# Performance work log

Hardware: AMD Instinct MI355X
Metric: run time of the kernel (lower is better)

Reference implementation:

```python
import jax, jax.numpy as jnp
import numpy as np

B, S, UNITS = 32, 2048, 512
D = 2 * UNITS  # 1024


def setup_inputs() -> dict:
    key = jax.random.key(0)
    ks = jax.random.split(key, 12)
    s = 1.0 / np.sqrt(D)
    mask = (jax.random.uniform(ks[0], (B, S)) < 0.9).astype(jnp.float32)
    mask = mask.at[:, 0].set(1.0)  # guarantee no all-zero row
    return {
        "dec_hidden": jax.random.normal(ks[1], (2, B, UNITS), dtype=jnp.float32),
        "enc_output": jax.random.normal(ks[2], (B, S, D), dtype=jnp.float32),
        "enc_pad_mask": mask,
        "prev_coverage": jax.random.uniform(ks[3], (B, S), dtype=jnp.float32) * 0.1,
        "Wh": jax.random.uniform(ks[4], (D, D), minval=-s, maxval=s),
        "bh": jax.random.uniform(ks[5], (D,), minval=-s, maxval=s),
        "Ws": jax.random.uniform(ks[6], (D, D), minval=-s, maxval=s),
        "bs": jax.random.uniform(ks[7], (D,), minval=-s, maxval=s),
        "Wc": jax.random.uniform(ks[8], (D, 1), minval=-1.0, maxval=1.0),
        "bc": jax.random.uniform(ks[9], (D,), minval=-1.0, maxval=1.0),
        "v": jax.random.uniform(ks[10], (1, D), minval=-s, maxval=s),
        "bv": jax.random.uniform(ks[11], (1,), minval=-s, maxval=s),
        "use_coverage": 1,
    }


def reference(dec_hidden, enc_output, enc_pad_mask, prev_coverage,
              Wh, bh, Ws, bs, Wc, bc, v, bv, use_coverage):
    # dec_hidden: (2, B, units) -> (B, 1, 2*units)
    dec = jnp.transpose(dec_hidden, (1, 0, 2)).reshape(dec_hidden.shape[1], 1, -1)
    enc_features = jnp.einsum('bsd,ed->bse', enc_output, Wh) + bh  # (B,S,D)
    dec_features = jnp.einsum('bod,ed->boe', dec, Ws) + bs          # (B,1,D)
    att_inputs = enc_features + dec_features
    if use_coverage:
        # Linear(1 -> D) applied to prev_coverage[..., None]
        coverage_features = prev_coverage[:, :, None] * Wc[:, 0][None, None, :] + bc
        att_inputs = att_inputs + coverage_features
    score = jnp.einsum('bsd,od->bso', jnp.tanh(att_inputs), v) + bv  # (B,S,1)
    attention_weights = jax.nn.softmax(score, axis=1)[..., 0]        # (B,S)
    attention_weights = attention_weights * enc_pad_mask
    attention_weights = attention_weights / jnp.sum(attention_weights, axis=1, keepdims=True)
    context_vector = jnp.einsum('bs,bsd->bd', attention_weights, enc_output)
    if use_coverage:
        coverage_vector = prev_coverage + attention_weights
        return context_vector, attention_weights, coverage_vector
    return context_vector, attention_weights
```

## Files before the change

kernel.cpp:

```cpp
#include <hip/hip_runtime.h>
#include <hip/hip_bf16.h>

#define BATCH 32
#define SEQ   2048
#define DIM   1024

typedef __attribute__((ext_vector_type(4))) float f32x4;
typedef __attribute__((ext_vector_type(8))) short short8;

static __device__ __forceinline__ ushort f2bf(float x) {
    __hip_bfloat16 h = __float2bfloat16(x);
    union { __hip_bfloat16 h; ushort u; } cv; cv.h = h;
    return cv.u;
}

__global__ __launch_bounds__(256) void kWhPack(const float* __restrict__ Wh,
                                               ushort* __restrict__ whbp) {
    int g = blockIdx.x * 256 + threadIdx.x;
    int l  = g & 63;
    int kb = (g >> 6) & 31;
    int eb = g >> 11;
    int e  = eb * 16 + (l & 15);
    int k0 = kb * 32 + (l >> 4) * 8;
    const float* src = Wh + (size_t)e * DIM + k0;
    float4 a = *(const float4*)src;
    float4 b = *(const float4*)(src + 4);
    union { ushort us[8]; uint4 u4; } pk;
    pk.us[0] = f2bf(a.x); pk.us[1] = f2bf(a.y); pk.us[2] = f2bf(a.z); pk.us[3] = f2bf(a.w);
    pk.us[4] = f2bf(b.x); pk.us[5] = f2bf(b.y); pk.us[6] = f2bf(b.z); pk.us[7] = f2bf(b.w);
    *(uint4*)(whbp + (size_t)g * 8) = pk.u4;
}

__global__ __launch_bounds__(256) void kBase(const float* __restrict__ dh,
                                             const float* __restrict__ Ws,
                                             const float* __restrict__ bs,
                                             const float* __restrict__ bh,
                                             const float* __restrict__ bc,
                                             const int* __restrict__ uc,
                                             float* __restrict__ base) {
    __shared__ float dec[8][DIM];
    int ec = blockIdx.x >> 2;
    int bg = blockIdx.x & 3;
    int b0 = bg * 8, e0 = ec * 32;
    int tid = threadIdx.x;
    for (int i = tid; i < 8 * DIM; i += 256) {
        int bb = i >> 10, d = i & 1023;
        float vdec = (d < 512) ? dh[(b0 + bb) * 512 + d]
                               : dh[BATCH * 512 + (b0 + bb) * 512 + d - 512];
        dec[bb][d] = vdec;
    }
    __syncthreads();
    int el = tid >> 3, ds = tid & 7;
    int e = e0 + el;
    float acc[8] = {0.f, 0.f, 0.f, 0.f, 0.f, 0.f, 0.f, 0.f};
    const float* wrow = Ws + (size_t)e * DIM;
    for (int i = 0; i < 128; ++i) {
        int d = i * 8 + ds;
        float wv = wrow[d];
#pragma unroll
        for (int bb = 0; bb < 8; ++bb) acc[bb] += wv * dec[bb][d];
    }
#pragma unroll
    for (int bb = 0; bb < 8; ++bb) {
        float s = acc[bb];
        s += __shfl_xor(s, 1); s += __shfl_xor(s, 2); s += __shfl_xor(s, 4);
        acc[bb] = s;
    }
    if (ds == 0) {
        float bias = bs[e] + bh[e] + ((*uc) ? bc[e] : 0.0f);
#pragma unroll
        for (int bb = 0; bb < 8; ++bb) base[(b0 + bb) * DIM + e] = acc[bb] + bias;
    }
}

__global__ __launch_bounds__(1024, 4) void kScore(const float* __restrict__ enc,
                                                  const ushort* __restrict__ whbp,
                                                  const float* __restrict__ base,
                                                  const float* __restrict__ pc,
                                                  const float* __restrict__ Wc,
                                                  const float* __restrict__ vv,
                                                  const int* __restrict__ uc,
                                                  float* __restrict__ score) {
    __shared__ ushort lds[2][64 * 128];
    __shared__ float pcl[64];
    __shared__ float red[16][64];

    const int tid = threadIdx.x;
    const int w = tid >> 6;
    const int lane = tid & 63;
    const int q = lane >> 4, l15 = lane & 15;
    const int bx = blockIdx.x;
    const int b = bx >> 5;
    const int s0 = (bx & 31) << 6;

    const float* Ab = enc + ((size_t)(b * SEQ + s0)) * DIM;
    if (tid < 64) pcl[tid] = pc[b * SEQ + s0 + tid];

    const int srow = tid >> 4;
    const int sslot = tid & 15;
    const int swidx = srow * 128 + (((sslot ^ (srow & 15))) << 3);
    const float* gsrc = Ab + (size_t)srow * DIM + (sslot << 3);

    f32x4 acc[4][4] = {};

    {
        float4 a0 = *(const float4*)gsrc;
        float4 a1 = *(const float4*)(gsrc + 4);
        union { ushort us[8]; uint4 u4; } pk;
        pk.us[0] = f2bf(a0.x); pk.us[1] = f2bf(a0.y); pk.us[2] = f2bf(a0.z); pk.us[3] = f2bf(a0.w);
        pk.us[4] = f2bf(a1.x); pk.us[5] = f2bf(a1.y); pk.us[6] = f2bf(a1.z); pk.us[7] = f2bf(a1.w);
        *(uint4*)(&lds[0][swidx]) = pk.u4;
    }
    __syncthreads();

    for (int kt = 0; kt < 8; ++kt) {
        float4 a0, a1;
        if (kt < 7) {
            a0 = *(const float4*)(gsrc + (kt + 1) * 128);
            a1 = *(const float4*)(gsrc + (kt + 1) * 128 + 4);
        }
        const ushort* Lb = lds[kt & 1];
#pragma unroll
        for (int kk = 0; kk < 128; kk += 32) {
            short8 bfr[4];
#pragma unroll
            for (int ef = 0; ef < 4; ++ef) {
                int fidx = (((w << 2) + ef) << 5) + (kt << 2) + (kk >> 5);
                bfr[ef] = *(const short8*)(whbp + ((size_t)fidx << 9) + (lane << 3));
            }
            short8 af[4];
#pragma unroll
            for (int mf = 0; mf < 4; ++mf) {
                int idx = ((mf << 4) + l15) * 128 + ((kk + (q << 3)) ^ (l15 << 3));
                af[mf] = *(const short8*)(&Lb[idx]);
            }
#pragma unroll
            for (int ef = 0; ef < 4; ++ef)
#pragma unroll
                for (int mf = 0; mf < 4; ++mf)
                    acc[mf][ef] = __builtin_amdgcn_mfma_f32_16x16x32_bf16(af[mf], bfr[ef], acc[mf][ef], 0, 0, 0);
        }
        if (kt < 7) {
            union { ushort us[8]; uint4 u4; } pk;
            pk.us[0] = f2bf(a0.x); pk.us[1] = f2bf(a0.y); pk.us[2] = f2bf(a0.z); pk.us[3] = f2bf(a0.w);
            pk.us[4] = f2bf(a1.x); pk.us[5] = f2bf(a1.y); pk.us[6] = f2bf(a1.z); pk.us[7] = f2bf(a1.w);
            *(uint4*)(&lds[(kt + 1) & 1][swidx]) = pk.u4;
        }
        __syncthreads();
    }

    const float ucf = (float)(*uc);
    float basee[4], ve[4], wce[4];
#pragma unroll
    for (int ef = 0; ef < 4; ++ef) {
        int e = (w << 6) + (ef << 4) + l15;
        basee[ef] = base[b * DIM + e];
        ve[ef] = vv[e];
        wce[ef] = Wc[e] * ucf;
    }
#pragma unroll
    for (int mf = 0; mf < 4; ++mf) {
#pragma unroll
        for (int r = 0; r < 4; ++r) {
            int rl = (mf << 4) + (q << 2) + r;
            float p = pcl[rl];
            float sp = 0.f;
#pragma unroll
            for (int ef = 0; ef < 4; ++ef) {
                float x = acc[mf][ef][r] + basee[ef] + p * wce[ef];
                float t = 1.0f - 2.0f / (1.0f + __expf(2.0f * x));
                sp += t * ve[ef];
            }
            sp += __shfl_xor(sp, 1);
            sp += __shfl_xor(sp, 2);
            sp += __shfl_xor(sp, 4);
            sp += __shfl_xor(sp, 8);
            if (l15 == 0) red[w][rl] = sp;
        }
    }
    __syncthreads();
    if (tid < 64) {
        float s = 0.f;
#pragma unroll
        for (int ww = 0; ww < 16; ++ww) s += red[ww][tid];
        score[b * SEQ + s0 + tid] = s;
    }
}

__global__ __launch_bounds__(512) void kSoftmax(const float* __restrict__ score,
                                                const float* __restrict__ mask,
                                                const float* __restrict__ pc,
                                                float* __restrict__ att,
                                                float* __restrict__ cov,
                                                int write_cov) {
    __shared__ float rmax[8], rsum[8];
    int b = blockIdx.x, tid = threadIdx.x;
    int wv = tid >> 6, ln = tid & 63;
    float x[4];
#pragma unroll
    for (int i = 0; i < 4; ++i) x[i] = score[b * SEQ + tid + i * 512];
    float m = fmaxf(fmaxf(x[0], x[1]), fmaxf(x[2], x[3]));
#pragma unroll
    for (int o = 1; o < 64; o <<= 1) m = fmaxf(m, __shfl_xor(m, o));
    if (ln == 0) rmax[wv] = m;
    __syncthreads();
    m = rmax[0];
#pragma unroll
    for (int i = 1; i < 8; ++i) m = fmaxf(m, rmax[i]);

    float ms[4], wm[4];
#pragma unroll
    for (int i = 0; i < 4; ++i) ms[i] = mask[b * SEQ + tid + i * 512];
    float s = 0.f;
#pragma unroll
    for (int i = 0; i < 4; ++i) { wm[i] = __expf(x[i] - m) * ms[i]; s += wm[i]; }
#pragma unroll
    for (int o = 1; o < 64; o <<= 1) s += __shfl_xor(s, o);
    if (ln == 0) rsum[wv] = s;
    __syncthreads();
    s = 0.f;
#pragma unroll
    for (int i = 0; i < 8; ++i) s += rsum[i];
    float inv = 1.0f / s;
#pragma unroll
    for (int i = 0; i < 4; ++i) {
        float wf = wm[i] * inv;
        att[b * SEQ + tid + i * 512] = wf;
        if (write_cov) cov[b * SEQ + tid + i * 512] = pc[b * SEQ + tid + i * 512] + wf;
    }
}

__global__ __launch_bounds__(256) void kCtxPart(const float* __restrict__ enc,
                                                const float* __restrict__ att,
                                                float* __restrict__ part) {
    __shared__ float wl[64];
    int bx = blockIdx.x;
    int b = bx >> 5, sc = bx & 31;
    int tid = threadIdx.x;
    if (tid < 64) wl[tid] = att[b * SEQ + sc * 64 + tid];
    __syncthreads();
    const float* basep = enc + ((size_t)(b * SEQ + sc * 64)) * DIM + tid * 4;
    float4 acc = {0.f, 0.f, 0.f, 0.f};
#pragma unroll 4
    for (int i = 0; i < 64; ++i) {
        float w = wl[i];
        float4 xv = *(const float4*)(basep + (size_t)i * DIM);
        acc.x += w * xv.x; acc.y += w * xv.y; acc.z += w * xv.z; acc.w += w * xv.w;
    }
    *(float4*)(part + (size_t)bx * DIM + tid * 4) = acc;
}

__global__ __launch_bounds__(256) void kCtxReduce(const float* __restrict__ part,
                                                  float* __restrict__ ctx) {
    int g = blockIdx.x * 256 + threadIdx.x;
    int b = g >> 10, d = g & 1023;
    float s = 0.f;
#pragma unroll
    for (int i = 0; i < 32; ++i) s += part[((size_t)(b * 32 + i) << 10) + d];
    ctx[g] = s;
}

extern "C" void kernel_launch(void* const* d_in, const int* in_sizes, int n_in,
                              void* d_out, int out_size, void* d_ws, size_t ws_size,
                              hipStream_t stream) {
    const float* dh   = (const float*)d_in[0];
    const float* enc  = (const float*)d_in[1];
    const float* mask = (const float*)d_in[2];
    const float* pc   = (const float*)d_in[3];
    const float* Wh   = (const float*)d_in[4];
    const float* bh   = (const float*)d_in[5];
    const float* Ws   = (const float*)d_in[6];
    const float* bs   = (const float*)d_in[7];
    const float* Wc   = (const float*)d_in[8];
    const float* bc   = (const float*)d_in[9];
    const float* vv   = (const float*)d_in[10];
    const int* uc     = (const int*)d_in[12];

    float* ctx = (float*)d_out;
    float* att = ctx + BATCH * DIM;
    float* cov = att + BATCH * SEQ;
    int write_cov = (out_size >= BATCH * (DIM + 2 * SEQ)) ? 1 : 0;

    ushort* whbp = (ushort*)d_ws;
    float* base  = (float*)((char*)d_ws + 2u * 1024u * 1024u);
    float* score = base + BATCH * DIM;
    float* part  = score + BATCH * SEQ;

    kWhPack<<<512, 256, 0, stream>>>(Wh, whbp);
    kBase<<<128, 256, 0, stream>>>(dh, Ws, bs, bh, bc, uc, base);
    kScore<<<1024, 1024, 0, stream>>>(enc, whbp, base, pc, Wc, vv, uc, score);
    kSoftmax<<<BATCH, 512, 0, stream>>>(score, mask, pc, att, cov, write_cov);
    kCtxPart<<<1024, 256, 0, stream>>>(enc, att, part);
    kCtxReduce<<<128, 256, 0, stream>>>(part, ctx);
}
```

Measured before the change: 281.1 us.

## Retile score GEMM to 128x512 blocks with LDS-staged Wh via global_load_lds

Each score block now covers 128 sequence rows and half of the output features, in place of 64 rows and all 1024 features. The Wh tiles are staged into LDS with direct global-to-LDS loads, and the K-loop steps 32 wide over 32 iterations with padded A rows. Because each block produces only half of each score, kScore writes two partial score buffers and the softmax kernel sums them. The aim is to cut redundant per-wave global reads of Wh and improve reuse. The cost is more loop iterations and barriers, extra LDS use and a larger workspace.

```diff
diff --git a/kernel.cpp b/kernel.cpp
--- a/kernel.cpp
+++ b/kernel.cpp
@@ -7,11 +7,18 @@
 
 typedef __attribute__((ext_vector_type(4))) float f32x4;
 typedef __attribute__((ext_vector_type(8))) short short8;
+typedef __attribute__((ext_vector_type(4))) ushort u16x4;
 
 static __device__ __forceinline__ ushort f2bf(float x) {
     __hip_bfloat16 h = __float2bfloat16(x);
     union { __hip_bfloat16 h; ushort u; } cv; cv.h = h;
     return cv.u;
+}
+
+static __device__ __forceinline__ void gll16(const void* g, void* l) {
+    __builtin_amdgcn_global_load_lds(
+        (const __attribute__((address_space(1))) void*)g,
+        (__attribute__((address_space(3))) void*)l, 16, 0, 0);
 }
 
 __global__ __launch_bounds__(256) void kWhPack(const float* __restrict__ Wh,
@@ -80,80 +87,81 @@
                                                   const float* __restrict__ Wc,
                                                   const float* __restrict__ vv,
                                                   const int* __restrict__ uc,
-                                                  float* __restrict__ score) {
-    __shared__ ushort lds[2][64 * 128];
-    __shared__ float pcl[64];
+                                                  float* __restrict__ scorep) {
+    __shared__ ushort Bl[2][16384];
+    __shared__ ushort Al[2][128 * 40];
+    __shared__ float pcl[128];
     __shared__ float red[16][64];
 
     const int tid = threadIdx.x;
     const int w = tid >> 6;
     const int lane = tid & 63;
     const int q = lane >> 4, l15 = lane & 15;
-    const int bx = blockIdx.x;
-    const int b = bx >> 5;
-    const int s0 = (bx & 31) << 6;
+    const int wm = w >> 3, wn = w & 7;
+
+    const int hb = blockIdx.x;
+    const int nq = (hb >> 3) & 1;
+    const int rg = ((hb >> 4) << 3) + (hb & 7);
+    const int b = rg >> 4;
+    const int s0 = (rg & 15) << 7;
 
     const float* Ab = enc + ((size_t)(b * SEQ + s0)) * DIM;
-    if (tid < 64) pcl[tid] = pc[b * SEQ + s0 + tid];
-
-    const int srow = tid >> 4;
-    const int sslot = tid & 15;
-    const int swidx = srow * 128 + (((sslot ^ (srow & 15))) << 3);
-    const float* gsrc = Ab + (size_t)srow * DIM + (sslot << 3);
+    if (tid < 128) pcl[tid] = pc[b * SEQ + s0 + tid];
+
+    const int arow = tid >> 3, ak4 = (tid & 7) << 2;
+    const float* agsrc = Ab + (size_t)arow * DIM + ak4;
+    const int awidx = arow * 40 + ak4;
+
+    const int ebg0 = nq * 32 + w * 2;
+    const ushort* bgsrc0 = whbp + ((size_t)(ebg0 + 0) << 14) + (lane << 3);
+    const ushort* bgsrc1 = whbp + ((size_t)(ebg0 + 1) << 14) + (lane << 3);
+    ushort* bdst0_base0 = &Bl[0][(w * 2 + 0) * 512];
+    ushort* bdst1_base0 = &Bl[0][(w * 2 + 1) * 512];
 
     f32x4 acc[4][4] = {};
 
     {
-        float4 a0 = *(const float4*)gsrc;
-        float4 a1 = *(const float4*)(gsrc + 4);
-        union { ushort us[8]; uint4 u4; } pk;
-        pk.us[0] = f2bf(a0.x); pk.us[1] = f2bf(a0.y); pk.us[2] = f2bf(a0.z); pk.us[3] = f2bf(a0.w);
-        pk.us[4] = f2bf(a1.x); pk.us[5] = f2bf(a1.y); pk.us[6] = f2bf(a1.z); pk.us[7] = f2bf(a1.w);
-        *(uint4*)(&lds[0][swidx]) = pk.u4;
-    }
-    __syncthreads();
-
-    for (int kt = 0; kt < 8; ++kt) {
-        float4 a0, a1;
-        if (kt < 7) {
-            a0 = *(const float4*)(gsrc + (kt + 1) * 128);
-            a1 = *(const float4*)(gsrc + (kt + 1) * 128 + 4);
+        gll16(bgsrc0, bdst0_base0);
+        gll16(bgsrc1, bdst1_base0);
+        float4 a4 = *(const float4*)agsrc;
+        u16x4 p; p[0] = f2bf(a4.x); p[1] = f2bf(a4.y); p[2] = f2bf(a4.z); p[3] = f2bf(a4.w);
+        *(u16x4*)&Al[0][awidx] = p;
+    }
+    __syncthreads();
+
+    int buf = 0;
+    for (int kt = 0; kt < 32; ++kt) {
+        float4 a4;
+        if (kt < 31) {
+            gll16(bgsrc0 + ((size_t)(kt + 1) << 9), &Bl[buf ^ 1][(w * 2 + 0) * 512]);
+            gll16(bgsrc1 + ((size_t)(kt + 1) << 9), &Bl[buf ^ 1][(w * 2 + 1) * 512]);
+            a4 = *(const float4*)(agsrc + (kt + 1) * 32);
         }
-        const ushort* Lb = lds[kt & 1];
-#pragma unroll
-        for (int kk = 0; kk < 128; kk += 32) {
-            short8 bfr[4];
-#pragma unroll
-            for (int ef = 0; ef < 4; ++ef) {
-                int fidx = (((w << 2) + ef) << 5) + (kt << 2) + (kk >> 5);
-                bfr[ef] = *(const short8*)(whbp + ((size_t)fidx << 9) + (lane << 3));
-            }
-            short8 af[4];
-#pragma unroll
-            for (int mf = 0; mf < 4; ++mf) {
-                int idx = ((mf << 4) + l15) * 128 + ((kk + (q << 3)) ^ (l15 << 3));
-                af[mf] = *(const short8*)(&Lb[idx]);
-            }
-#pragma unroll
-            for (int ef = 0; ef < 4; ++ef)
-#pragma unroll
-                for (int mf = 0; mf < 4; ++mf)
-                    acc[mf][ef] = __builtin_amdgcn_mfma_f32_16x16x32_bf16(af[mf], bfr[ef], acc[mf][ef], 0, 0, 0);
-        }
-        if (kt < 7) {
-            union { ushort us[8]; uint4 u4; } pk;
-            pk.us[0] = f2bf(a0.x); pk.us[1] = f2bf(a0.y); pk.us[2] = f2bf(a0.z); pk.us[3] = f2bf(a0.w);
-            pk.us[4] = f2bf(a1.x); pk.us[5] = f2bf(a1.y); pk.us[6] = f2bf(a1.z); pk.us[7] = f2bf(a1.w);
-            *(uint4*)(&lds[(kt + 1) & 1][swidx]) = pk.u4;
+        short8 af[4], bf[4];
+#pragma unroll
+        for (int mf = 0; mf < 4; ++mf)
+            af[mf] = *(const short8*)&Al[buf][(wm * 64 + mf * 16 + l15) * 40 + q * 8];
+#pragma unroll
+        for (int ef = 0; ef < 4; ++ef)
+            bf[ef] = *(const short8*)&Bl[buf][(wn * 4 + ef) * 512 + lane * 8];
+#pragma unroll
+        for (int ef = 0; ef < 4; ++ef)
+#pragma unroll
+            for (int mf = 0; mf < 4; ++mf)
+                acc[mf][ef] = __builtin_amdgcn_mfma_f32_16x16x32_bf16(af[mf], bf[ef], acc[mf][ef], 0, 0, 0);
+        if (kt < 31) {
+            u16x4 p; p[0] = f2bf(a4.x); p[1] = f2bf(a4.y); p[2] = f2bf(a4.z); p[3] = f2bf(a4.w);
+            *(u16x4*)&Al[buf ^ 1][awidx] = p;
         }
         __syncthreads();
+        buf ^= 1;
     }
 
     const float ucf = (float)(*uc);
     float basee[4], ve[4], wce[4];
 #pragma unroll
     for (int ef = 0; ef < 4; ++ef) {
-        int e = (w << 6) + (ef << 4) + l15;
+        int e = nq * 512 + wn * 64 + ef * 16 + l15;
         basee[ef] = base[b * DIM + e];
         ve[ef] = vv[e];
         wce[ef] = Wc[e] * ucf;
@@ -163,7 +171,7 @@
 #pragma unroll
         for (int r = 0; r < 4; ++r) {
             int rl = (mf << 4) + (q << 2) + r;
-            float p = pcl[rl];
+            float p = pcl[wm * 64 + rl];
             float sp = 0.f;
 #pragma unroll
             for (int ef = 0; ef < 4; ++ef) {
@@ -179,15 +187,16 @@
         }
     }
     __syncthreads();
-    if (tid < 64) {
+    if (tid < 128) {
+        int wmf = tid >> 6, rl = tid & 63;
         float s = 0.f;
 #pragma unroll
-        for (int ww = 0; ww < 16; ++ww) s += red[ww][tid];
-        score[b * SEQ + s0 + tid] = s;
-    }
-}
-
-__global__ __launch_bounds__(512) void kSoftmax(const float* __restrict__ score,
+        for (int j = 0; j < 8; ++j) s += red[wmf * 8 + j][rl];
+        scorep[nq * (BATCH * SEQ) + b * SEQ + s0 + tid] = s;
+    }
+}
+
+__global__ __launch_bounds__(512) void kSoftmax(const float* __restrict__ scorep,
                                                 const float* __restrict__ mask,
                                                 const float* __restrict__ pc,
                                                 float* __restrict__ att,
@@ -198,7 +207,10 @@
     int wv = tid >> 6, ln = tid & 63;
     float x[4];
 #pragma unroll
-    for (int i = 0; i < 4; ++i) x[i] = score[b * SEQ + tid + i * 512];
+    for (int i = 0; i < 4; ++i) {
+        int idx = b * SEQ + tid + i * 512;
+        x[i] = scorep[idx] + scorep[BATCH * SEQ + idx];
+    }
     float m = fmaxf(fmaxf(x[0], x[1]), fmaxf(x[2], x[3]));
 #pragma unroll
     for (int o = 1; o < 64; o <<= 1) m = fmaxf(m, __shfl_xor(m, o));
@@ -281,15 +293,15 @@
     float* cov = att + BATCH * SEQ;
     int write_cov = (out_size >= BATCH * (DIM + 2 * SEQ)) ? 1 : 0;
 
-    ushort* whbp = (ushort*)d_ws;
-    float* base  = (float*)((char*)d_ws + 2u * 1024u * 1024u);
-    float* score = base + BATCH * DIM;
-    float* part  = score + BATCH * SEQ;
+    ushort* whbp  = (ushort*)d_ws;
+    float* base   = (float*)((char*)d_ws + 2u * 1024u * 1024u);
+    float* scorep = base + BATCH * DIM;
+    float* part   = scorep + 2 * BATCH * SEQ;
 
     kWhPack<<<512, 256, 0, stream>>>(Wh, whbp);
     kBase<<<128, 256, 0, stream>>>(dh, Ws, bs, bh, bc, uc, base);
-    kScore<<<1024, 1024, 0, stream>>>(enc, whbp, base, pc, Wc, vv, uc, score);
-    kSoftmax<<<BATCH, 512, 0, stream>>>(score, mask, pc, att, cov, write_cov);
+    kScore<<<1024, 1024, 0, stream>>>(enc, whbp, base, pc, Wc, vv, uc, scorep);
+    kSoftmax<<<BATCH, 512, 0, stream>>>(scorep, mask, pc, att, cov, write_cov);
     kCtxPart<<<1024, 256, 0, stream>>>(enc, att, part);
     kCtxReduce<<<128, 256, 0, stream>>>(part, ctx);
 }
```

Result: faster. 270.5 us (-3.8%).
